# Performance work log

Hardware: AMD Instinct MI355X
Metric: run time of the kernel (lower is better)

## Reference

```python
import jax, jax.numpy as jnp
import numpy as np

NQ = 4      # n_qubits
T = 512     # seq_lenght
H = 1024    # hidden_size
F = 64      # input feature size
B = 16      # batch size (hardcoded in original module)


def _circuit_tables(nq):
    idx = np.arange(2 ** nq)
    # BasicEntanglerLayers CNOT ring: (0,1),(1,2),...,(n-1,0) for n>2; single CNOT for n==2
    pairs = [(i, (i + 1) % nq) for i in range(nq)] if nq > 2 else [(0, 1)]
    perms = []
    for c, t in pairs:  # CNOT as a basis-state permutation (qubit 0 = MSB)
        ctrl = (idx >> (nq - 1 - c)) & 1
        perms.append(idx ^ (ctrl << (nq - 1 - t)))
    bits = (idx[:, None] >> (nq - 1 - np.arange(nq))[None, :]) & 1
    signs = (1.0 - 2.0 * bits).astype(np.float32)  # (2**nq, nq), <Z_q> signs
    return perms, signs

_PERMS, _SIGNS = _circuit_tables(NQ)
_SIGNS_J = jnp.asarray(_SIGNS)


def circuit_expvals(theta):
    """theta: (..., NQ) total RX angle per wire (AngleEmbedding RX + entangler RX).
    Returns (..., NQ) PauliZ expvals after product-RX state + CNOT ring."""
    half = 0.5 * theta
    a0 = jnp.cos(half).astype(jnp.complex64)
    a1 = (-1j * jnp.sin(half)).astype(jnp.complex64)
    state = jnp.ones(theta.shape[:-1] + (1,), dtype=jnp.complex64)
    for q in range(NQ):  # build product state, qubit 0 most significant
        amp = jnp.stack([a0[..., q], a1[..., q]], axis=-1)
        state = (state[..., :, None] * amp[..., None, :]).reshape(theta.shape[:-1] + (-1,))
    for perm in _PERMS:  # CNOT ring = permutations of the computational basis
        state = state[..., perm]
    probs = state.real ** 2 + state.imag ** 2  # (..., 2**NQ)
    return probs @ _SIGNS_J                     # (..., NQ)


def qlstm_last(x, w4, Wy, by, Wf, bf, Wi, bi, Wu, bu, Wo, bo):
    """x: (B, T, feat). Dense params are stacked per-timestep along axis 0 (T,...)
    (the original creates a fresh nn.Dense every loop iteration).
    Returns the hidden state at the last timestep, (B, H)."""
    h0 = jnp.zeros((x.shape[0], H), dtype=x.dtype)
    c0 = jnp.zeros((x.shape[0], H), dtype=x.dtype)

    def step(carry, inp):
        h, c = carry
        x_t, wy, byt, wf, bft, wi, bit_, wu, but, wo, bot = inp
        v = jnp.concatenate([h, x_t], axis=1)
        y = v @ wy + byt                                   # (B, NQ)
        z = circuit_expvals(y[None] + w4[:, None, :])      # (4, B, NQ), shared input, 4 gate weights
        f = jax.nn.sigmoid(z[0]) @ wf + bft                # NOTE: no activation after Dense, as in source
        i = jax.nn.sigmoid(z[1]) @ wi + bit_
        g = jnp.tanh(z[2]) @ wu + but
        o = jax.nn.sigmoid(z[3]) @ wo + bot
        c = f * c + i * g
        h = o * jnp.tanh(c)
        return (h, c), None

    xs = (jnp.swapaxes(x, 0, 1), Wy, by, Wf, bf, Wi, bi, Wu, bu, Wo, bo)
    (h, _), _ = jax.lax.scan(step, (h0, c0), xs)
    return h


def setup_inputs() -> dict:
    key = jax.random.key(0)
    ks = jax.random.split(key, 16)
    def w(k, shape, fan_in):
        return jax.random.normal(k, shape, jnp.float32) / np.sqrt(fan_in)
    inp = {"x": jax.random.normal(ks[0], (B, T, F), jnp.float32)}
    # quantum weights (n_qlayers=1, n_qubits) per gate
    for n, k in zip(["qwf", "qwi", "qwu", "qwo"], jax.random.split(ks[1], 4)):
        inp[n] = jax.random.uniform(k, (1, NQ), jnp.float32, -1.0, 1.0)
    # encoder: per-timestep Dense stacks
    inp["Wy_e"] = w(ks[2], (T, H + F, NQ), H + F); inp["by_e"] = jnp.zeros((T, NQ), jnp.float32)
    for n, k in zip(["f", "i", "u", "o"], jax.random.split(ks[3], 4)):
        inp["W" + n + "_e"] = w(k, (T, NQ, H), NQ)
        inp["b" + n + "_e"] = jnp.zeros((T, H), jnp.float32)
    # decoder: input feature size 1
    inp["Wy_d"] = w(ks[4], (T, H + 1, NQ), H + 1); inp["by_d"] = jnp.zeros((T, NQ), jnp.float32)
    for n, k in zip(["f", "i", "u", "o"], jax.random.split(ks[5], 4)):
        inp["W" + n + "_d"] = w(k, (T, NQ, H), NQ)
        inp["b" + n + "_d"] = jnp.zeros((T, H), jnp.float32)
    # final Dense(seq_lenght)
    inp["Wt"] = w(ks[6], (H, T), H); inp["bt"] = jnp.zeros((T,), jnp.float32)
    return inp


def reference(x, qwf, qwi, qwu, qwo,
              Wy_e, by_e, Wf_e, bf_e, Wi_e, bi_e, Wu_e, bu_e, Wo_e, bo_e,
              Wy_d, by_d, Wf_d, bf_d, Wi_d, bi_d, Wu_d, bu_d, Wo_d, bo_d,
              Wt, bt):
    w4 = jnp.stack([qwf[0], qwi[0], qwu[0], qwo[0]])  # only layer-0 row is used by the qnode
    h_enc = qlstm_last(x, w4, Wy_e, by_e, Wf_e, bf_e, Wi_e, bi_e, Wu_e, bu_e, Wo_e, bo_e)
    x2 = h_enc[:, :, None]                 # (B, H, 1)
    h_dec = qlstm_last(x2[:, :T, :], w4, Wy_d, by_d, Wf_d, bf_d, Wi_d, bi_d, Wu_d, bu_d, Wo_d, bo_d)
    target = h_dec @ Wt + bt               # (B, T)
    return target[:, :, None]              # (B, T, 1)
```

## Files before the change

kernel.cpp:

```cpp
#include <hip/hip_runtime.h>

#define Tn 512
#define Hn 1024
#define Fn 64
#define NTH 512
#define NW (NTH / 64)

#define STEPB (6u * 512u * 16u)
#define MAXTOFF (511u * STEPB)
#define REC_PASS ((unsigned long long)Tn * STEPB)
#define YXE_OFF (2ull * REC_PASS)
#define WS_NEED (2ull * REC_PASS + 16ull * 512ull * 16ull)

typedef unsigned u32x4 __attribute__((ext_vector_type(4)));
typedef __fp16 h2 __attribute__((ext_vector_type(2)));

struct QParams {
  const float *x;
  const float *qw0, *qw1, *qw2, *qw3;
  const float *Wy_e, *by_e, *Wf_e, *bf_e, *Wi_e, *bi_e, *Wu_e, *bu_e, *Wo_e, *bo_e;
  const float *Wy_d, *by_d, *Wf_d, *bf_d, *Wi_d, *bi_d, *Wu_d, *bu_d, *Wo_d, *bo_d;
  const float *Wt, *bt;
  float *out;
};

#define BAR()                                                                  \
  do {                                                                         \
    asm volatile("s_waitcnt lgkmcnt(0)" ::: "memory");                         \
    __builtin_amdgcn_s_barrier();                                              \
    asm volatile("" ::: "memory");                                             \
  } while (0)
#define WAIT_VM(N)                                                             \
  do {                                                                         \
    asm volatile("s_waitcnt vmcnt(" #N ")" ::: "memory");                      \
    __builtin_amdgcn_sched_barrier(0);                                         \
  } while (0)

template <int CTRL, int RM, int BM, bool BC>
__device__ __forceinline__ float dppadd(float x) {
  int t = __builtin_amdgcn_update_dpp(0, __builtin_bit_cast(int, x), CTRL, RM,
                                      BM, BC);
  return x + __builtin_bit_cast(float, t);
}
template <int CTRL>
__device__ __forceinline__ float dppmov(float x) {
  int t = __builtin_amdgcn_update_dpp(0, __builtin_bit_cast(int, x), CTRL, 0xF,
                                      0xF, true);
  return __builtin_bit_cast(float, t);
}
__device__ __forceinline__ float wave_sum63(float x) {
  x = dppadd<0xB1, 0xF, 0xF, true>(x);
  x = dppadd<0x4E, 0xF, 0xF, true>(x);
  x = dppadd<0x141, 0xF, 0xF, true>(x);
  x = dppadd<0x140, 0xF, 0xF, true>(x);
  x = dppadd<0x142, 0xA, 0xF, false>(x);
  x = dppadd<0x143, 0xC, 0xF, false>(x);
  return x;
}
__device__ __forceinline__ float tanhc(float c) {
  float e = __builtin_amdgcn_exp2f(c * 2.885390081777927f);
  return fmaf(-2.f, __builtin_amdgcn_rcpf(e + 1.f), 1.f);
}
__device__ __forceinline__ h2 pk2(float a, float b) {
  return __builtin_amdgcn_cvt_pkrtz(a, b);
}
__device__ __forceinline__ h2 uh(unsigned u) { return __builtin_bit_cast(h2, u); }
__device__ __forceinline__ float fdot2f(h2 a, h2 b, float c) {
#if __has_builtin(__builtin_amdgcn_fdot2)
  return __builtin_amdgcn_fdot2(a, b, c, false);
#else
  float d;
  asm("v_dot2_f32_f16 %0, %1, %2, %3" : "=v"(d) : "v"(a), "v"(b), "v"(c));
  return d;
#endif
}
__device__ __forceinline__ unsigned pkh(float a, float b) {
  h2 h;
  h.x = (__fp16)a;
  h.y = (__fp16)b;
  return __builtin_bit_cast(unsigned, h);
}

struct LaneCtx {
  int tid, lane, wid;
  unsigned jt16;
  bool q1, q2;
  float w4lane;
  float mlane, alane, klane;
};
struct SBase {
  unsigned long long a[6];
};

__global__ __launch_bounds__(512) void qprep_kernel(QParams p, char *ws) {
  int t = blockIdx.x;
  const bool dec = (t >= 512);
  if (dec) t -= 512;
  const int j = threadIdx.x;

  const float *Wg0 = dec ? p.Wf_d : p.Wf_e, *Wg1 = dec ? p.Wi_d : p.Wi_e;
  const float *Wg2 = dec ? p.Wu_d : p.Wu_e, *Wg3 = dec ? p.Wo_d : p.Wo_e;
  const float *bf = dec ? p.bf_d : p.bf_e, *bi = dec ? p.bi_d : p.bi_e;
  const float *bu = dec ? p.bu_d : p.bu_e, *bo = dec ? p.bo_d : p.bo_e;
  const float *Wy = dec ? p.Wy_d : p.Wy_e;
  const int K = dec ? (Hn + 1) : (Hn + Fn);

  u32x4 *dst = (u32x4 *)(ws + (dec ? REC_PASS : 0));
  const int rbase = t * 6 * 512 + j;
  const int t4 = t * 4096;
  const float *Wg[4] = {Wg0, Wg1, Wg2, Wg3};
#pragma unroll
  for (int g = 0; g < 4; ++g) {
    u32x4 v;
    v.x = pkh(Wg[g][t4 + 0 * 1024 + j], Wg[g][t4 + 1 * 1024 + j]);
    v.y = pkh(Wg[g][t4 + 2 * 1024 + j], Wg[g][t4 + 3 * 1024 + j]);
    v.z = pkh(Wg[g][t4 + 0 * 1024 + j + 512], Wg[g][t4 + 1 * 1024 + j + 512]);
    v.w = pkh(Wg[g][t4 + 2 * 1024 + j + 512], Wg[g][t4 + 3 * 1024 + j + 512]);
    dst[rbase + g * 512] = v;
  }
  {
    const int tb = t * 1024;
    u32x4 v = {pkh(bf[tb + j], bf[tb + j + 512]),
               pkh(bi[tb + j], bi[tb + j + 512]),
               pkh(bu[tb + j], bu[tb + j + 512]),
               pkh(bo[tb + j], bo[tb + j + 512])};
    dst[rbase + 4 * 512] = v;
  }
  {
    const float4 w0 = *(const float4 *)(Wy + ((size_t)t * K + j) * 4);
    const float4 w1 = *(const float4 *)(Wy + ((size_t)t * K + j + 512) * 4);
    u32x4 v = {pkh(w0.x, w1.x), pkh(w0.y, w1.y), pkh(w0.z, w1.z),
               pkh(w0.w, w1.w)};
    dst[rbase + 5 * 512] = v;
  }

  if (!dec && j < 16) {
    const int b = j;
    float a0 = p.by_e[t * 4 + 0], a1 = p.by_e[t * 4 + 1],
          a2 = p.by_e[t * 4 + 2], a3 = p.by_e[t * 4 + 3];
#pragma unroll 8
    for (int k = 0; k < 64; ++k) {
      const float xv = p.x[((size_t)b * Tn + t) * Fn + k];
      const float4 wr =
          *(const float4 *)(p.Wy_e + ((size_t)t * (Hn + Fn) + Hn + k) * 4);
      a0 = fmaf(xv, wr.x, a0);
      a1 = fmaf(xv, wr.y, a1);
      a2 = fmaf(xv, wr.z, a2);
      a3 = fmaf(xv, wr.w, a3);
    }
    ((float4 *)(ws + YXE_OFF))[(size_t)b * Tn + t] =
        make_float4(a0, a1, a2, a3);
  }
}

struct Regs {
  u32x4 c0, c1, c2, c3, c4, c5;
};

__device__ __forceinline__ void issue_pf(Regs &r, const SBase &sb,
                                         unsigned voff) {
  asm volatile("global_load_dwordx4 %0, %1, %2" : "=v"(r.c5) : "v"(voff), "s"(sb.a[5]));
  asm volatile("global_load_dwordx4 %0, %1, %2" : "=v"(r.c0) : "v"(voff), "s"(sb.a[0]));
  asm volatile("global_load_dwordx4 %0, %1, %2" : "=v"(r.c1) : "v"(voff), "s"(sb.a[1]));
  asm volatile("global_load_dwordx4 %0, %1, %2" : "=v"(r.c2) : "v"(voff), "s"(sb.a[2]));
  asm volatile("global_load_dwordx4 %0, %1, %2" : "=v"(r.c3) : "v"(voff), "s"(sb.a[3]));
  asm volatile("global_load_dwordx4 %0, %1, %2" : "=v"(r.c4) : "v"(voff), "s"(sb.a[4]));
}

template <int PAR>
__device__ __forceinline__ void
qstep(int t, Regs &r, unsigned &toff, const SBase &sb, const LaneCtx &L,
      float *red_t, const float *yxby_l, float &h0, float &h1, float &c0,
      float &c1, h2 &hp) {
  const float yxs = yxby_l[t * 4 + (L.lane & 3)];
  WAIT_VM(18);
  float a0 = fdot2f(hp, uh(r.c5.x), 0.f);
  float a1 = fdot2f(hp, uh(r.c5.y), 0.f);
  float a2 = fdot2f(hp, uh(r.c5.z), 0.f);
  float a3 = fdot2f(hp, uh(r.c5.w), 0.f);
  a0 = wave_sum63(a0);
  a1 = wave_sum63(a1);
  a2 = wave_sum63(a2);
  a3 = wave_sum63(a3);
  if (L.lane == 63) {
    red_t[PAR * 32 + 0 * 8 + L.wid] = a0;
    red_t[PAR * 32 + 1 * 8 + L.wid] = a1;
    red_t[PAR * 32 + 2 * 8 + L.wid] = a2;
    red_t[PAR * 32 + 3 * 8 + L.wid] = a3;
  }
  BAR();
  const float4 rA = *(const float4 *)&red_t[PAR * 32 + (L.lane & 3) * 8 + 0];
  const float4 rB = *(const float4 *)&red_t[PAR * 32 + (L.lane & 3) * 8 + 4];
  const float yq =
      ((rA.x + rA.y) + (rA.z + rA.w)) + ((rB.x + rB.y) + (rB.z + rB.w));
  const float ang = yq + yxs + L.w4lane;
  const float cc = __cosf(ang);
  const float t1 = dppmov<0xB1>(cc);
  const float d1 = cc * t1;
  const float t2 = dppmov<0x4E>(d1);
  const float d2 = d1 * t2;
  const float zu = t1 * t2;
  const float zv = cc * t2;
  const float z = L.q2 ? (L.q1 ? d2 : zv) : (L.q1 ? d1 : zu);
  const float s =
      __builtin_amdgcn_rcpf(1.f + __builtin_amdgcn_exp2f(L.klane * z));
  const float act = fmaf(s, L.mlane, L.alane);
  const float actn = dppmov<0xB1>(act);
  const unsigned apk = __builtin_bit_cast(unsigned, pk2(act, actn));
  const h2 F01 = uh((unsigned)__builtin_amdgcn_readlane(apk, 0));
  const h2 F23 = uh((unsigned)__builtin_amdgcn_readlane(apk, 2));
  const h2 I01 = uh((unsigned)__builtin_amdgcn_readlane(apk, 4));
  const h2 I23 = uh((unsigned)__builtin_amdgcn_readlane(apk, 6));
  const h2 U01 = uh((unsigned)__builtin_amdgcn_readlane(apk, 8));
  const h2 U23 = uh((unsigned)__builtin_amdgcn_readlane(apk, 10));
  const h2 O01 = uh((unsigned)__builtin_amdgcn_readlane(apk, 12));
  const h2 O23 = uh((unsigned)__builtin_amdgcn_readlane(apk, 14));
  const h2 bgf = uh(r.c4.x), bgi = uh(r.c4.y), bgu = uh(r.c4.z),
           bgo = uh(r.c4.w);
  const float fv0 = fdot2f(F01, uh(r.c0.x), fdot2f(F23, uh(r.c0.y), (float)bgf.x));
  const float fv1 = fdot2f(F01, uh(r.c0.z), fdot2f(F23, uh(r.c0.w), (float)bgf.y));
  const float iv0 = fdot2f(I01, uh(r.c1.x), fdot2f(I23, uh(r.c1.y), (float)bgi.x));
  const float iv1 = fdot2f(I01, uh(r.c1.z), fdot2f(I23, uh(r.c1.w), (float)bgi.y));
  const float uv0 = fdot2f(U01, uh(r.c2.x), fdot2f(U23, uh(r.c2.y), (float)bgu.x));
  const float uv1 = fdot2f(U01, uh(r.c2.z), fdot2f(U23, uh(r.c2.w), (float)bgu.y));
  const float ov0 = fdot2f(O01, uh(r.c3.x), fdot2f(O23, uh(r.c3.y), (float)bgo.x));
  const float ov1 = fdot2f(O01, uh(r.c3.z), fdot2f(O23, uh(r.c3.w), (float)bgo.y));
  c0 = fmaf(fv0, c0, iv0 * uv0);
  h0 = ov0 * tanhc(c0);
  c1 = fmaf(fv1, c1, iv1 * uv1);
  h1 = ov1 * tanhc(c1);
  hp = pk2(h0, h1);
  issue_pf(r, sb, L.jt16 + toff);
  toff = toff + STEPB;
  if (toff > MAXTOFF) toff = MAXTOFF;
}

__device__ __forceinline__ void run_pass(const SBase &sb, const LaneCtx &L,
                                         float *red_t, const float *yxby_l,
                                         float &h0, float &h1, float &c0,
                                         float &c1) {
  Regs R0, R1, R2, R3;
  issue_pf(R0, sb, L.jt16 + 0 * STEPB);
  issue_pf(R1, sb, L.jt16 + 1 * STEPB);
  issue_pf(R2, sb, L.jt16 + 2 * STEPB);
  issue_pf(R3, sb, L.jt16 + 3 * STEPB);
  unsigned toff = 4 * STEPB;
  h2 hp = pk2(0.f, 0.f);
  for (int t = 0; t < Tn; t += 4) {
    qstep<0>(t + 0, R0, toff, sb, L, red_t, yxby_l, h0, h1, c0, c1, hp);
    qstep<1>(t + 1, R1, toff, sb, L, red_t, yxby_l, h0, h1, c0, c1, hp);
    qstep<0>(t + 2, R2, toff, sb, L, red_t, yxby_l, h0, h1, c0, c1, hp);
    qstep<1>(t + 3, R3, toff, sb, L, red_t, yxby_l, h0, h1, c0, c1, hp);
  }
  asm volatile("s_waitcnt vmcnt(0)" ::: "memory");
  __builtin_amdgcn_sched_barrier(0);
}

__global__ __launch_bounds__(NTH, 2) void qlstm_f16_kernel(QParams p,
                                                           char *ws) {
  const int b = blockIdx.x;
  LaneCtx L;
  L.tid = threadIdx.x;
  L.lane = L.tid & 63;
  L.wid = L.tid >> 6;
  L.jt16 = (unsigned)L.tid * 16u;
  const int q = L.lane & 3, g = (L.lane >> 2) & 3;
  L.q1 = q & 1;
  L.q2 = q & 2;
  {
    const float *qwp =
        (g == 0) ? p.qw0 : (g == 1) ? p.qw1 : (g == 2) ? p.qw2 : p.qw3;
    L.w4lane = qwp[q];
  }
  L.mlane = (g == 2) ? 2.f : 1.f;
  L.alane = 1.f - L.mlane;
  L.klane = -L.mlane * 1.4426950408889634f;

  __shared__ __align__(16) float red_t[2 * 4 * 8];
  __shared__ __align__(16) float yxby_l[Tn * 4];
  __shared__ __align__(16) float hbuf[Hn];

  SBase sbE, sbD;
#pragma unroll
  for (int k = 0; k < 6; ++k) {
    sbE.a[k] = (unsigned long long)ws + (unsigned long long)k * 8192ull;
    sbD.a[k] = (unsigned long long)ws + REC_PASS + (unsigned long long)k * 8192ull;
  }

  ((float4 *)yxby_l)[L.tid] =
      ((const float4 *)(ws + YXE_OFF))[(size_t)b * Tn + L.tid];
  float h0 = 0.f, h1 = 0.f, c0 = 0.f, c1 = 0.f;
  __syncthreads();

  run_pass(sbE, L, red_t, yxby_l, h0, h1, c0, c1);

  __syncthreads();
  hbuf[L.tid] = h0;
  hbuf[L.tid + NTH] = h1;
  __syncthreads();
  {
    const float hv = hbuf[L.tid];
    const float4 wx =
        *(const float4 *)(p.Wy_d + ((size_t)L.tid * (Hn + 1) + Hn) * 4);
    const float4 bd = *(const float4 *)(p.by_d + L.tid * 4);
    ((float4 *)yxby_l)[L.tid] =
        make_float4(fmaf(hv, wx.x, bd.x), fmaf(hv, wx.y, bd.y),
                    fmaf(hv, wx.z, bd.z), fmaf(hv, wx.w, bd.w));
  }
  h0 = h1 = c0 = c1 = 0.f;
  __syncthreads();

  run_pass(sbD, L, red_t, yxby_l, h0, h1, c0, c1);

  __syncthreads();
  hbuf[L.tid] = h0;
  hbuf[L.tid + NTH] = h1;
  __syncthreads();
  {
    float acc = p.bt[L.tid];
    const float4 *h4 = (const float4 *)hbuf;
#pragma unroll 4
    for (int j4 = 0; j4 < Hn / 4; ++j4) {
      const float4 hv = h4[j4];
      acc = fmaf(hv.x, p.Wt[(j4 * 4 + 0) * Tn + L.tid], acc);
      acc = fmaf(hv.y, p.Wt[(j4 * 4 + 1) * Tn + L.tid], acc);
      acc = fmaf(hv.z, p.Wt[(j4 * 4 + 2) * Tn + L.tid], acc);
      acc = fmaf(hv.w, p.Wt[(j4 * 4 + 3) * Tn + L.tid], acc);
    }
    p.out[(size_t)b * Tn + L.tid] = acc;
  }
}

__device__ __forceinline__ float sum8_all(float x) {
  x = dppadd<0xB1, 0xF, 0xF, true>(x);
  x = dppadd<0x4E, 0xF, 0xF, true>(x);
  x = dppadd<0x141, 0xF, 0xF, true>(x);
  return x;
}

struct WB {
  float w[32];
  float bb[8];
  float4 wy0, wy1;
  float4 wyx;
  float xv;
};

template <bool DEC>
__device__ __forceinline__ WB
pf_fb(int t, int b, int tid, const float *__restrict__ x,
      const float *__restrict__ Wy, const float *__restrict__ Wf,
      const float *__restrict__ bfp, const float *__restrict__ Wi,
      const float *__restrict__ bip, const float *__restrict__ Wu,
      const float *__restrict__ bup, const float *__restrict__ Wo,
      const float *__restrict__ bop) {
  WB d;
  const int K = DEC ? (Hn + 1) : (Hn + Fn);
  const int g0 = t * 4096 + tid;
#pragma unroll
  for (int e = 0; e < 2; ++e) {
    const int ge = g0 + e * 512;
#pragma unroll
    for (int n = 0; n < 4; ++n) {
      d.w[e * 16 + 0 * 4 + n] = Wf[ge + n * 1024];
      d.w[e * 16 + 1 * 4 + n] = Wi[ge + n * 1024];
      d.w[e * 16 + 2 * 4 + n] = Wu[ge + n * 1024];
      d.w[e * 16 + 3 * 4 + n] = Wo[ge + n * 1024];
    }
    const int be = t * 1024 + tid + e * 512;
    d.bb[e * 4 + 0] = bfp[be];
    d.bb[e * 4 + 1] = bip[be];
    d.bb[e * 4 + 2] = bup[be];
    d.bb[e * 4 + 3] = bop[be];
  }
  d.wy0 = *(const float4 *)(Wy + (t * K + tid) * 4);
  d.wy1 = *(const float4 *)(Wy + (t * K + tid + 512) * 4);
  if (!DEC) {
    if (tid < Fn) {
      d.wyx = *(const float4 *)(Wy + (t * K + Hn + tid) * 4);
      d.xv = x[(b * Tn + t) * Fn + tid];
    }
  } else {
    if (tid == 0) d.wyx = *(const float4 *)(Wy + (t * K + Hn) * 4);
  }
  return d;
}

template <bool DEC, int PAR>
__device__ __forceinline__ void
step_fb(int t, int tn, const WB &rd, WB &wr, int b, const LaneCtx &L,
        const float *__restrict__ x, const float *__restrict__ Wy,
        const float *__restrict__ Wf, const float *__restrict__ bfp,
        const float *__restrict__ Wi, const float *__restrict__ bip,
        const float *__restrict__ Wu, const float *__restrict__ bup,
        const float *__restrict__ Wo, const float *__restrict__ bop,
        float4 (*red4)[NW], const float *by_l, const float *henc_s, float &h0,
        float &h1, float &c0, float &c1) {
  float a0 = h0 * rd.wy0.x, a1 = h0 * rd.wy0.y, a2 = h0 * rd.wy0.z,
        a3 = h0 * rd.wy0.w;
  a0 = fmaf(h1, rd.wy1.x, a0);
  a1 = fmaf(h1, rd.wy1.y, a1);
  a2 = fmaf(h1, rd.wy1.z, a2);
  a3 = fmaf(h1, rd.wy1.w, a3);
  if (!DEC) {
    if (L.tid < Fn) {
      a0 = fmaf(rd.xv, rd.wyx.x, a0);
      a1 = fmaf(rd.xv, rd.wyx.y, a1);
      a2 = fmaf(rd.xv, rd.wyx.z, a2);
      a3 = fmaf(rd.xv, rd.wyx.w, a3);
    }
  } else {
    if (L.tid == 0) {
      const float xv = henc_s[t];
      a0 = fmaf(xv, rd.wyx.x, a0);
      a1 = fmaf(xv, rd.wyx.y, a1);
      a2 = fmaf(xv, rd.wyx.z, a2);
      a3 = fmaf(xv, rd.wyx.w, a3);
    }
  }
  a0 = wave_sum63(a0);
  a1 = wave_sum63(a1);
  a2 = wave_sum63(a2);
  a3 = wave_sum63(a3);
  if (L.lane == 63) red4[PAR][L.wid] = make_float4(a0, a1, a2, a3);
  wr = pf_fb<DEC>(tn, b, L.tid, x, Wy, Wf, bfp, Wi, bip, Wu, bup, Wo, bop);
  BAR();
  float4 rv = red4[PAR][L.lane & 7];
  const float byq = by_l[t * 4 + (L.lane & 3)];
  float y0 = sum8_all(rv.x), y1 = sum8_all(rv.y), y2 = sum8_all(rv.z),
        y3 = sum8_all(rv.w);
  const float yq = L.q2 ? (L.q1 ? y3 : y2) : (L.q1 ? y1 : y0);
  const float ang = yq + byq + L.w4lane;
  const float cc = __cosf(ang);
  const float t1 = dppmov<0xB1>(cc);
  const float d1 = cc * t1;
  const float t2 = dppmov<0x4E>(d1);
  const float d2 = d1 * t2;
  const float zu = t1 * t2;
  const float zv = cc * t2;
  const float z = L.q2 ? (L.q1 ? d2 : zv) : (L.q1 ? d1 : zu);
  const float s =
      __builtin_amdgcn_rcpf(1.f + __builtin_amdgcn_exp2f(L.klane * z));
  const float act = fmaf(s, L.mlane, L.alane);
#define RL(n)                                                                  \
  __builtin_bit_cast(float,                                                    \
                     __builtin_amdgcn_readlane(__builtin_bit_cast(int, act), n))
  const float f0 = RL(0), f1 = RL(1), f2 = RL(2), f3 = RL(3);
  const float i0 = RL(4), i1 = RL(5), i2 = RL(6), i3 = RL(7);
  const float u0 = RL(8), u1 = RL(9), u2 = RL(10), u3 = RL(11);
  const float o0 = RL(12), o1 = RL(13), o2 = RL(14), o3 = RL(15);
#undef RL
#pragma unroll
  for (int e = 0; e < 2; ++e) {
    float fv = rd.bb[e * 4 + 0], iv = rd.bb[e * 4 + 1], uv = rd.bb[e * 4 + 2],
          ov = rd.bb[e * 4 + 3];
    fv = fmaf(f0, rd.w[e * 16 + 0], fv);
    fv = fmaf(f1, rd.w[e * 16 + 1], fv);
    fv = fmaf(f2, rd.w[e * 16 + 2], fv);
    fv = fmaf(f3, rd.w[e * 16 + 3], fv);
    iv = fmaf(i0, rd.w[e * 16 + 4], iv);
    iv = fmaf(i1, rd.w[e * 16 + 5], iv);
    iv = fmaf(i2, rd.w[e * 16 + 6], iv);
    iv = fmaf(i3, rd.w[e * 16 + 7], iv);
    uv = fmaf(u0, rd.w[e * 16 + 8], uv);
    uv = fmaf(u1, rd.w[e * 16 + 9], uv);
    uv = fmaf(u2, rd.w[e * 16 + 10], uv);
    uv = fmaf(u3, rd.w[e * 16 + 11], uv);
    ov = fmaf(o0, rd.w[e * 16 + 12], ov);
    ov = fmaf(o1, rd.w[e * 16 + 13], ov);
    ov = fmaf(o2, rd.w[e * 16 + 14], ov);
    ov = fmaf(o3, rd.w[e * 16 + 15], ov);
    float &cr = e ? c1 : c0;
    float &hr = e ? h1 : h0;
    const float cn = fmaf(fv, cr, iv * uv);
    cr = cn;
    hr = ov * tanhc(cn);
  }
}

template <bool DEC>
__device__ void lstm_pass_fb(int b, const LaneCtx &L,
                             const float *__restrict__ x,
                             const float *__restrict__ Wy,
                             const float *__restrict__ by,
                             const float *__restrict__ Wf,
                             const float *__restrict__ bfp,
                             const float *__restrict__ Wi,
                             const float *__restrict__ bip,
                             const float *__restrict__ Wu,
                             const float *__restrict__ bup,
                             const float *__restrict__ Wo,
                             const float *__restrict__ bop,
                             float4 (*red4)[NW], float *by_l,
                             const float *henc_s, float &h0, float &h1,
                             float &c0, float &c1) {
#pragma unroll
  for (int i = 0; i < (Tn * 4) / NTH; ++i)
    by_l[L.tid + i * NTH] = by[L.tid + i * NTH];
  __syncthreads();
  WB bufA = pf_fb<DEC>(0, b, L.tid, x, Wy, Wf, bfp, Wi, bip, Wu, bup, Wo, bop);
  WB bufB;
  for (int t = 0; t < Tn; t += 2) {
    step_fb<DEC, 0>(t, t + 1, bufA, bufB, b, L, x, Wy, Wf, bfp, Wi, bip, Wu,
                    bup, Wo, bop, red4, by_l, henc_s, h0, h1, c0, c1);
    step_fb<DEC, 1>(t + 1, (t + 2 < Tn) ? (t + 2) : (Tn - 1), bufB, bufA, b, L,
                    x, Wy, Wf, bfp, Wi, bip, Wu, bup, Wo, bop, red4, by_l,
                    henc_s, h0, h1, c0, c1);
  }
}

__global__ __launch_bounds__(NTH, 2) void qlstm_fb_kernel(QParams p) {
  const int b = blockIdx.x;
  LaneCtx L;
  L.tid = threadIdx.x;
  L.lane = L.tid & 63;
  L.wid = L.tid >> 6;
  L.jt16 = (unsigned)L.tid * 16u;
  const int q = L.lane & 3, g = (L.lane >> 2) & 3;
  L.q1 = q & 1;
  L.q2 = q & 2;
  {
    const float *qwp =
        (g == 0) ? p.qw0 : (g == 1) ? p.qw1 : (g == 2) ? p.qw2 : p.qw3;
    L.w4lane = qwp[q];
  }
  L.mlane = (g == 2) ? 2.f : 1.f;
  L.alane = 1.f - L.mlane;
  L.klane = -L.mlane * 1.4426950408889634f;

  __shared__ float4 red4[2][NW];
  __shared__ float by_l[Tn * 4];
  __shared__ float henc_s[Hn];
  __shared__ float hst[Hn];

  float h0 = 0.f, h1 = 0.f, c0 = 0.f, c1 = 0.f;

  lstm_pass_fb<false>(b, L, p.x, p.Wy_e, p.by_e, p.Wf_e, p.bf_e, p.Wi_e,
                      p.bi_e, p.Wu_e, p.bu_e, p.Wo_e, p.bo_e, red4, by_l,
                      henc_s, h0, h1, c0, c1);
  henc_s[L.tid] = h0;
  henc_s[L.tid + NTH] = h1;
  h0 = h1 = c0 = c1 = 0.f;
  __syncthreads();
  lstm_pass_fb<true>(b, L, nullptr, p.Wy_d, p.by_d, p.Wf_d, p.bf_d, p.Wi_d,
                     p.bi_d, p.Wu_d, p.bu_d, p.Wo_d, p.bo_d, red4, by_l,
                     henc_s, h0, h1, c0, c1);
  hst[L.tid] = h0;
  hst[L.tid + NTH] = h1;
  __syncthreads();
  {
    float acc = p.bt[L.tid];
    const float4 *h4 = (const float4 *)hst;
#pragma unroll 4
    for (int j4 = 0; j4 < Hn / 4; ++j4) {
      const float4 hv = h4[j4];
      acc = fmaf(hv.x, p.Wt[(j4 * 4 + 0) * Tn + L.tid], acc);
      acc = fmaf(hv.y, p.Wt[(j4 * 4 + 1) * Tn + L.tid], acc);
      acc = fmaf(hv.z, p.Wt[(j4 * 4 + 2) * Tn + L.tid], acc);
      acc = fmaf(hv.w, p.Wt[(j4 * 4 + 3) * Tn + L.tid], acc);
    }
    p.out[(size_t)b * Tn + L.tid] = acc;
  }
}

extern "C" void kernel_launch(void *const *d_in, const int *in_sizes, int n_in,
                              void *d_out, int out_size, void *d_ws,
                              size_t ws_size, hipStream_t stream) {
  QParams p;
  p.x = (const float *)d_in[0];
  p.qw0 = (const float *)d_in[1];
  p.qw1 = (const float *)d_in[2];
  p.qw2 = (const float *)d_in[3];
  p.qw3 = (const float *)d_in[4];
  p.Wy_e = (const float *)d_in[5];
  p.by_e = (const float *)d_in[6];
  p.Wf_e = (const float *)d_in[7];
  p.bf_e = (const float *)d_in[8];
  p.Wi_e = (const float *)d_in[9];
  p.bi_e = (const float *)d_in[10];
  p.Wu_e = (const float *)d_in[11];
  p.bu_e = (const float *)d_in[12];
  p.Wo_e = (const float *)d_in[13];
  p.bo_e = (const float *)d_in[14];
  p.Wy_d = (const float *)d_in[15];
  p.by_d = (const float *)d_in[16];
  p.Wf_d = (const float *)d_in[17];
  p.bf_d = (const float *)d_in[18];
  p.Wi_d = (const float *)d_in[19];
  p.bi_d = (const float *)d_in[20];
  p.Wu_d = (const float *)d_in[21];
  p.bu_d = (const float *)d_in[22];
  p.Wo_d = (const float *)d_in[23];
  p.bo_d = (const float *)d_in[24];
  p.Wt = (const float *)d_in[25];
  p.bt = (const float *)d_in[26];
  p.out = (float *)d_out;

  if (ws_size >= WS_NEED) {
    char *ws = (char *)d_ws;
    hipLaunchKernelGGL(qprep_kernel, dim3(1024), dim3(512), 0, stream, p, ws);
    hipLaunchKernelGGL(qlstm_f16_kernel, dim3(16), dim3(NTH), 0, stream, p,
                       ws);
  } else {
    hipLaunchKernelGGL(qlstm_fb_kernel, dim3(16), dim3(NTH), 0, stream, p);
  }
}
```

Before: 691.0 us.

## Skip gate-bias stream when all biases are zero and fold 2π into weights

```diff
diff --git a/kernel.cpp b/kernel.cpp
--- a/kernel.cpp
+++ b/kernel.cpp
@@ -6,11 +6,15 @@
 #define NTH 512
 #define NW (NTH / 64)
 
-#define STEPB (6u * 512u * 16u)
+#define STEPB (5u * 512u * 16u)
 #define MAXTOFF (511u * STEPB)
+#define MAXBOFF (511u * 4096u)
 #define REC_PASS ((unsigned long long)Tn * STEPB)
 #define YXE_OFF (2ull * REC_PASS)
-#define WS_NEED (2ull * REC_PASS + 16ull * 512ull * 16ull)
+#define FLAG_OFF (YXE_OFF + 131072ull)
+#define WS_NEED (FLAG_OFF + 64ull)
+
+#define INV2PI 0.15915494309189535f
 
 typedef unsigned u32x4 __attribute__((ext_vector_type(4)));
 typedef __fp16 h2 __attribute__((ext_vector_type(2)));
@@ -74,6 +78,13 @@
   return d;
 #endif
 }
+__device__ __forceinline__ float cosrev(float x) {
+#if __has_builtin(__builtin_amdgcn_cosf)
+  return __builtin_amdgcn_cosf(x);
+#else
+  return __cosf(x * 6.283185307179586f);
+#endif
+}
 __device__ __forceinline__ unsigned pkh(float a, float b) {
   h2 h;
   h.x = (__fp16)a;
@@ -83,14 +94,18 @@
 
 struct LaneCtx {
   int tid, lane, wid;
-  unsigned jt16;
+  unsigned jt16, jt4;
   bool q1, q2;
-  float w4lane;
   float mlane, alane, klane;
 };
 struct SBase {
-  unsigned long long a[6];
+  unsigned long long a[5];
 };
+struct BBase {
+  unsigned long long b[4];
+};
+
+__global__ void qflag0_kernel(char *ws) { *(int *)(ws + FLAG_OFF) = 0; }
 
 __global__ __launch_bounds__(512) void qprep_kernel(QParams p, char *ws) {
   int t = blockIdx.x;
@@ -105,8 +120,7 @@
   const float *Wy = dec ? p.Wy_d : p.Wy_e;
   const int K = dec ? (Hn + 1) : (Hn + Fn);
 
-  u32x4 *dst = (u32x4 *)(ws + (dec ? REC_PASS : 0));
-  const int rbase = t * 6 * 512 + j;
+  char *base = ws + (dec ? REC_PASS : 0) + (size_t)t * STEPB;
   const int t4 = t * 4096;
   const float *Wg[4] = {Wg0, Wg1, Wg2, Wg3};
 #pragma unroll
@@ -116,22 +130,26 @@
     v.y = pkh(Wg[g][t4 + 2 * 1024 + j], Wg[g][t4 + 3 * 1024 + j]);
     v.z = pkh(Wg[g][t4 + 0 * 1024 + j + 512], Wg[g][t4 + 1 * 1024 + j + 512]);
     v.w = pkh(Wg[g][t4 + 2 * 1024 + j + 512], Wg[g][t4 + 3 * 1024 + j + 512]);
-    dst[rbase + g * 512] = v;
-  }
-  {
-    const int tb = t * 1024;
-    u32x4 v = {pkh(bf[tb + j], bf[tb + j + 512]),
-               pkh(bi[tb + j], bi[tb + j + 512]),
-               pkh(bu[tb + j], bu[tb + j + 512]),
-               pkh(bo[tb + j], bo[tb + j + 512])};
-    dst[rbase + 4 * 512] = v;
+    *(u32x4 *)(base + g * 8192 + j * 16) = v;
   }
   {
     const float4 w0 = *(const float4 *)(Wy + ((size_t)t * K + j) * 4);
     const float4 w1 = *(const float4 *)(Wy + ((size_t)t * K + j + 512) * 4);
-    u32x4 v = {pkh(w0.x, w1.x), pkh(w0.y, w1.y), pkh(w0.z, w1.z),
-               pkh(w0.w, w1.w)};
-    dst[rbase + 5 * 512] = v;
+    u32x4 v = {pkh(w0.x * INV2PI, w1.x * INV2PI),
+               pkh(w0.y * INV2PI, w1.y * INV2PI),
+               pkh(w0.z * INV2PI, w1.z * INV2PI),
+               pkh(w0.w * INV2PI, w1.w * INV2PI)};
+    *(u32x4 *)(base + 4 * 8192 + j * 16) = v;
+  }
+  {
+    const int tb = t * 1024 + j;
+    const float s0 = bf[tb], s1 = bf[tb + 512];
+    const float s2 = bi[tb], s3 = bi[tb + 512];
+    const float s4 = bu[tb], s5 = bu[tb + 512];
+    const float s6 = bo[tb], s7 = bo[tb + 512];
+    if (s0 != 0.f || s1 != 0.f || s2 != 0.f || s3 != 0.f || s4 != 0.f ||
+        s5 != 0.f || s6 != 0.f || s7 != 0.f)
+      atomicOr((int *)(ws + FLAG_OFF), 1);
   }
 
   if (!dec && j < 16) {
@@ -154,30 +172,47 @@
 }
 
 struct Regs {
-  u32x4 c0, c1, c2, c3, c4, c5;
+  u32x4 c0, c1, c2, c3;
+  u32x4 c4;
+  float bf0, bf1, bi0, bi1, bu0, bu1, bo0, bo1;
 };
 
+template <bool BIASED>
 __device__ __forceinline__ void issue_pf(Regs &r, const SBase &sb,
-                                         unsigned voff) {
-  asm volatile("global_load_dwordx4 %0, %1, %2" : "=v"(r.c5) : "v"(voff), "s"(sb.a[5]));
+                                         unsigned voff, const BBase &bb,
+                                         unsigned voffB) {
+  asm volatile("global_load_dwordx4 %0, %1, %2" : "=v"(r.c4) : "v"(voff), "s"(sb.a[4]));
   asm volatile("global_load_dwordx4 %0, %1, %2" : "=v"(r.c0) : "v"(voff), "s"(sb.a[0]));
   asm volatile("global_load_dwordx4 %0, %1, %2" : "=v"(r.c1) : "v"(voff), "s"(sb.a[1]));
   asm volatile("global_load_dwordx4 %0, %1, %2" : "=v"(r.c2) : "v"(voff), "s"(sb.a[2]));
   asm volatile("global_load_dwordx4 %0, %1, %2" : "=v"(r.c3) : "v"(voff), "s"(sb.a[3]));
-  asm volatile("global_load_dwordx4 %0, %1, %2" : "=v"(r.c4) : "v"(voff), "s"(sb.a[4]));
-}
-
-template <int PAR>
+  if (BIASED) {
+    asm volatile("global_load_dword %0, %1, %2" : "=v"(r.bf0) : "v"(voffB), "s"(bb.b[0]));
+    asm volatile("global_load_dword %0, %1, %2 offset:2048" : "=v"(r.bf1) : "v"(voffB), "s"(bb.b[0]));
+    asm volatile("global_load_dword %0, %1, %2" : "=v"(r.bi0) : "v"(voffB), "s"(bb.b[1]));
+    asm volatile("global_load_dword %0, %1, %2 offset:2048" : "=v"(r.bi1) : "v"(voffB), "s"(bb.b[1]));
+    asm volatile("global_load_dword %0, %1, %2" : "=v"(r.bu0) : "v"(voffB), "s"(bb.b[2]));
+    asm volatile("global_load_dword %0, %1, %2 offset:2048" : "=v"(r.bu1) : "v"(voffB), "s"(bb.b[2]));
+    asm volatile("global_load_dword %0, %1, %2" : "=v"(r.bo0) : "v"(voffB), "s"(bb.b[3]));
+    asm volatile("global_load_dword %0, %1, %2 offset:2048" : "=v"(r.bo1) : "v"(voffB), "s"(bb.b[3]));
+  }
+}
+
+template <int PAR, bool BIASED>
 __device__ __forceinline__ void
-qstep(int t, Regs &r, unsigned &toff, const SBase &sb, const LaneCtx &L,
-      float *red_t, const float *yxby_l, float &h0, float &h1, float &c0,
-      float &c1, h2 &hp) {
-  const float yxs = yxby_l[t * 4 + (L.lane & 3)];
-  WAIT_VM(18);
-  float a0 = fdot2f(hp, uh(r.c5.x), 0.f);
-  float a1 = fdot2f(hp, uh(r.c5.y), 0.f);
-  float a2 = fdot2f(hp, uh(r.c5.z), 0.f);
-  float a3 = fdot2f(hp, uh(r.c5.w), 0.f);
+qstep(int t, Regs &r, unsigned &toff, unsigned &toffB, const SBase &sb,
+      const BBase &bb, const LaneCtx &L, float *red_t, const float *yxw_l,
+      float &h0, float &h1, float &c0, float &c1, h2 &hp) {
+  const float yxw = yxw_l[t * 16 + (L.lane & 15)];
+  if (BIASED) {
+    WAIT_VM(39);
+  } else {
+    WAIT_VM(15);
+  }
+  float a0 = fdot2f(hp, uh(r.c4.x), 0.f);
+  float a1 = fdot2f(hp, uh(r.c4.y), 0.f);
+  float a2 = fdot2f(hp, uh(r.c4.z), 0.f);
+  float a3 = fdot2f(hp, uh(r.c4.w), 0.f);
   a0 = wave_sum63(a0);
   a1 = wave_sum63(a1);
   a2 = wave_sum63(a2);
@@ -193,8 +228,7 @@
   const float4 rB = *(const float4 *)&red_t[PAR * 32 + (L.lane & 3) * 8 + 4];
   const float yq =
       ((rA.x + rA.y) + (rA.z + rA.w)) + ((rB.x + rB.y) + (rB.z + rB.w));
-  const float ang = yq + yxs + L.w4lane;
-  const float cc = __cosf(ang);
+  const float cc = cosrev(yq + yxw);
   const float t1 = dppmov<0xB1>(cc);
   const float d1 = cc * t1;
   const float t2 = dppmov<0x4E>(d1);
@@ -215,42 +249,50 @@
   const h2 U23 = uh((unsigned)__builtin_amdgcn_readlane(apk, 10));
   const h2 O01 = uh((unsigned)__builtin_amdgcn_readlane(apk, 12));
   const h2 O23 = uh((unsigned)__builtin_amdgcn_readlane(apk, 14));
-  const h2 bgf = uh(r.c4.x), bgi = uh(r.c4.y), bgu = uh(r.c4.z),
-           bgo = uh(r.c4.w);
-  const float fv0 = fdot2f(F01, uh(r.c0.x), fdot2f(F23, uh(r.c0.y), (float)bgf.x));
-  const float fv1 = fdot2f(F01, uh(r.c0.z), fdot2f(F23, uh(r.c0.w), (float)bgf.y));
-  const float iv0 = fdot2f(I01, uh(r.c1.x), fdot2f(I23, uh(r.c1.y), (float)bgi.x));
-  const float iv1 = fdot2f(I01, uh(r.c1.z), fdot2f(I23, uh(r.c1.w), (float)bgi.y));
-  const float uv0 = fdot2f(U01, uh(r.c2.x), fdot2f(U23, uh(r.c2.y), (float)bgu.x));
-  const float uv1 = fdot2f(U01, uh(r.c2.z), fdot2f(U23, uh(r.c2.w), (float)bgu.y));
-  const float ov0 = fdot2f(O01, uh(r.c3.x), fdot2f(O23, uh(r.c3.y), (float)bgo.x));
-  const float ov1 = fdot2f(O01, uh(r.c3.z), fdot2f(O23, uh(r.c3.w), (float)bgo.y));
+  const float iF0 = BIASED ? r.bf0 : 0.f, iF1 = BIASED ? r.bf1 : 0.f;
+  const float iI0 = BIASED ? r.bi0 : 0.f, iI1 = BIASED ? r.bi1 : 0.f;
+  const float iU0 = BIASED ? r.bu0 : 0.f, iU1 = BIASED ? r.bu1 : 0.f;
+  const float iO0 = BIASED ? r.bo0 : 0.f, iO1 = BIASED ? r.bo1 : 0.f;
+  const float fv0 = fdot2f(F01, uh(r.c0.x), fdot2f(F23, uh(r.c0.y), iF0));
+  const float fv1 = fdot2f(F01, uh(r.c0.z), fdot2f(F23, uh(r.c0.w), iF1));
+  const float iv0 = fdot2f(I01, uh(r.c1.x), fdot2f(I23, uh(r.c1.y), iI0));
+  const float iv1 = fdot2f(I01, uh(r.c1.z), fdot2f(I23, uh(r.c1.w), iI1));
+  const float uv0 = fdot2f(U01, uh(r.c2.x), fdot2f(U23, uh(r.c2.y), iU0));
+  const float uv1 = fdot2f(U01, uh(r.c2.z), fdot2f(U23, uh(r.c2.w), iU1));
+  const float ov0 = fdot2f(O01, uh(r.c3.x), fdot2f(O23, uh(r.c3.y), iO0));
+  const float ov1 = fdot2f(O01, uh(r.c3.z), fdot2f(O23, uh(r.c3.w), iO1));
   c0 = fmaf(fv0, c0, iv0 * uv0);
   h0 = ov0 * tanhc(c0);
   c1 = fmaf(fv1, c1, iv1 * uv1);
   h1 = ov1 * tanhc(c1);
   hp = pk2(h0, h1);
-  issue_pf(r, sb, L.jt16 + toff);
+  issue_pf<BIASED>(r, sb, L.jt16 + toff, bb, L.jt4 + toffB);
   toff = toff + STEPB;
   if (toff > MAXTOFF) toff = MAXTOFF;
-}
-
-__device__ __forceinline__ void run_pass(const SBase &sb, const LaneCtx &L,
-                                         float *red_t, const float *yxby_l,
-                                         float &h0, float &h1, float &c0,
-                                         float &c1) {
+  if (BIASED) {
+    toffB = toffB + 4096u;
+    if (toffB > MAXBOFF) toffB = MAXBOFF;
+  }
+}
+
+template <bool BIASED>
+__device__ __forceinline__ void run_pass(const SBase &sb, const BBase &bb,
+                                         const LaneCtx &L, float *red_t,
+                                         const float *yxw_l, float &h0,
+                                         float &h1, float &c0, float &c1) {
   Regs R0, R1, R2, R3;
-  issue_pf(R0, sb, L.jt16 + 0 * STEPB);
-  issue_pf(R1, sb, L.jt16 + 1 * STEPB);
-  issue_pf(R2, sb, L.jt16 + 2 * STEPB);
-  issue_pf(R3, sb, L.jt16 + 3 * STEPB);
-  unsigned toff = 4 * STEPB;
+  WAIT_VM(0);
+  issue_pf<BIASED>(R0, sb, L.jt16 + 0 * STEPB, bb, L.jt4 + 0 * 4096u);
+  issue_pf<BIASED>(R1, sb, L.jt16 + 1 * STEPB, bb, L.jt4 + 1 * 4096u);
+  issue_pf<BIASED>(R2, sb, L.jt16 + 2 * STEPB, bb, L.jt4 + 2 * 4096u);
+  issue_pf<BIASED>(R3, sb, L.jt16 + 3 * STEPB, bb, L.jt4 + 3 * 4096u);
+  unsigned toff = 4 * STEPB, toffB = 4 * 4096u;
   h2 hp = pk2(0.f, 0.f);
   for (int t = 0; t < Tn; t += 4) {
-    qstep<0>(t + 0, R0, toff, sb, L, red_t, yxby_l, h0, h1, c0, c1, hp);
-    qstep<1>(t + 1, R1, toff, sb, L, red_t, yxby_l, h0, h1, c0, c1, hp);
-    qstep<0>(t + 2, R2, toff, sb, L, red_t, yxby_l, h0, h1, c0, c1, hp);
-    qstep<1>(t + 3, R3, toff, sb, L, red_t, yxby_l, h0, h1, c0, c1, hp);
+    qstep<0, BIASED>(t + 0, R0, toff, toffB, sb, bb, L, red_t, yxw_l, h0, h1, c0, c1, hp);
+    qstep<1, BIASED>(t + 1, R1, toff, toffB, sb, bb, L, red_t, yxw_l, h0, h1, c0, c1, hp);
+    qstep<0, BIASED>(t + 2, R2, toff, toffB, sb, bb, L, red_t, yxw_l, h0, h1, c0, c1, hp);
+    qstep<1, BIASED>(t + 3, R3, toff, toffB, sb, bb, L, red_t, yxw_l, h0, h1, c0, c1, hp);
   }
   asm volatile("s_waitcnt vmcnt(0)" ::: "memory");
   __builtin_amdgcn_sched_barrier(0);
@@ -264,35 +306,66 @@
   L.lane = L.tid & 63;
   L.wid = L.tid >> 6;
   L.jt16 = (unsigned)L.tid * 16u;
+  L.jt4 = (unsigned)L.tid * 4u;
   const int q = L.lane & 3, g = (L.lane >> 2) & 3;
   L.q1 = q & 1;
   L.q2 = q & 2;
-  {
-    const float *qwp =
-        (g == 0) ? p.qw0 : (g == 1) ? p.qw1 : (g == 2) ? p.qw2 : p.qw3;
-    L.w4lane = qwp[q];
-  }
   L.mlane = (g == 2) ? 2.f : 1.f;
   L.alane = 1.f - L.mlane;
   L.klane = -L.mlane * 1.4426950408889634f;
 
   __shared__ __align__(16) float red_t[2 * 4 * 8];
-  __shared__ __align__(16) float yxby_l[Tn * 4];
+  __shared__ __align__(16) float yxw_l[Tn * 16];
   __shared__ __align__(16) float hbuf[Hn];
 
+  const int biased = *(volatile const int *)(ws + FLAG_OFF);
+
   SBase sbE, sbD;
 #pragma unroll
-  for (int k = 0; k < 6; ++k) {
+  for (int k = 0; k < 5; ++k) {
     sbE.a[k] = (unsigned long long)ws + (unsigned long long)k * 8192ull;
     sbD.a[k] = (unsigned long long)ws + REC_PASS + (unsigned long long)k * 8192ull;
   }
-
-  ((float4 *)yxby_l)[L.tid] =
-      ((const float4 *)(ws + YXE_OFF))[(size_t)b * Tn + L.tid];
+  BBase bbE, bbD;
+  bbE.b[0] = (unsigned long long)p.bf_e;
+  bbE.b[1] = (unsigned long long)p.bi_e;
+  bbE.b[2] = (unsigned long long)p.bu_e;
+  bbE.b[3] = (unsigned long long)p.bo_e;
+  bbD.b[0] = (unsigned long long)p.bf_d;
+  bbD.b[1] = (unsigned long long)p.bi_d;
+  bbD.b[2] = (unsigned long long)p.bu_d;
+  bbD.b[3] = (unsigned long long)p.bo_d;
+
+  float4 w4r[4];
+  {
+    const float *qwp[4] = {p.qw0, p.qw1, p.qw2, p.qw3};
+#pragma unroll
+    for (int gg = 0; gg < 4; ++gg) {
+      const float4 w = *(const float4 *)qwp[gg];
+      w4r[gg] = make_float4(w.x * INV2PI, w.y * INV2PI, w.z * INV2PI,
+                            w.w * INV2PI);
+    }
+  }
+
+  {
+    const float4 yx4 =
+        ((const float4 *)(ws + YXE_OFF))[(size_t)b * Tn + L.tid];
+#pragma unroll
+    for (int gg = 0; gg < 4; ++gg) {
+      ((float4 *)yxw_l)[L.tid * 4 + gg] =
+          make_float4(fmaf(yx4.x, INV2PI, w4r[gg].x),
+                      fmaf(yx4.y, INV2PI, w4r[gg].y),
+                      fmaf(yx4.z, INV2PI, w4r[gg].z),
+                      fmaf(yx4.w, INV2PI, w4r[gg].w));
+    }
+  }
   float h0 = 0.f, h1 = 0.f, c0 = 0.f, c1 = 0.f;
   __syncthreads();
 
-  run_pass(sbE, L, red_t, yxby_l, h0, h1, c0, c1);
+  if (biased)
+    run_pass<true>(sbE, bbE, L, red_t, yxw_l, h0, h1, c0, c1);
+  else
+    run_pass<false>(sbE, bbE, L, red_t, yxw_l, h0, h1, c0, c1);
 
   __syncthreads();
   hbuf[L.tid] = h0;
@@ -303,14 +376,24 @@
     const float4 wx =
         *(const float4 *)(p.Wy_d + ((size_t)L.tid * (Hn + 1) + Hn) * 4);
     const float4 bd = *(const float4 *)(p.by_d + L.tid * 4);
-    ((float4 *)yxby_l)[L.tid] =
-        make_float4(fmaf(hv, wx.x, bd.x), fmaf(hv, wx.y, bd.y),
-                    fmaf(hv, wx.z, bd.z), fmaf(hv, wx.w, bd.w));
+    const float bx = fmaf(hv, wx.x, bd.x) * INV2PI;
+    const float by2 = fmaf(hv, wx.y, bd.y) * INV2PI;
+    const float bz = fmaf(hv, wx.z, bd.z) * INV2PI;
+    const float bw = fmaf(hv, wx.w, bd.w) * INV2PI;
+#pragma unroll
+    for (int gg = 0; gg < 4; ++gg) {
+      ((float4 *)yxw_l)[L.tid * 4 + gg] =
+          make_float4(bx + w4r[gg].x, by2 + w4r[gg].y, bz + w4r[gg].z,
+                      bw + w4r[gg].w);
+    }
   }
   h0 = h1 = c0 = c1 = 0.f;
   __syncthreads();
 
-  run_pass(sbD, L, red_t, yxby_l, h0, h1, c0, c1);
+  if (biased)
+    run_pass<true>(sbD, bbD, L, red_t, yxw_l, h0, h1, c0, c1);
+  else
+    run_pass<false>(sbD, bbD, L, red_t, yxw_l, h0, h1, c0, c1);
 
   __syncthreads();
   hbuf[L.tid] = h0;
@@ -331,6 +414,8 @@
   }
 }
 
+#define FNTH 512
+#define FNW (FNTH / 64)
 __device__ __forceinline__ float sum8_all(float x) {
   x = dppadd<0xB1, 0xF, 0xF, true>(x);
   x = dppadd<0x4E, 0xF, 0xF, true>(x);
@@ -386,15 +471,21 @@
   return d;
 }
 
+struct FLane {
+  int tid, lane, wid;
+  bool q1, q2;
+  float w4lane, mlane, alane, klane;
+};
+
 template <bool DEC, int PAR>
 __device__ __forceinline__ void
-step_fb(int t, int tn, const WB &rd, WB &wr, int b, const LaneCtx &L,
+step_fb(int t, int tn, const WB &rd, WB &wr, int b, const FLane &L,
         const float *__restrict__ x, const float *__restrict__ Wy,
         const float *__restrict__ Wf, const float *__restrict__ bfp,
         const float *__restrict__ Wi, const float *__restrict__ bip,
         const float *__restrict__ Wu, const float *__restrict__ bup,
         const float *__restrict__ Wo, const float *__restrict__ bop,
-        float4 (*red4)[NW], const float *by_l, const float *henc_s, float &h0,
+        float4 (*red4)[FNW], const float *by_l, const float *henc_s, float &h0,
         float &h1, float &c0, float &c1) {
   float a0 = h0 * rd.wy0.x, a1 = h0 * rd.wy0.y, a2 = h0 * rd.wy0.z,
         a3 = h0 * rd.wy0.w;
@@ -479,7 +570,7 @@
 }
 
 template <bool DEC>
-__device__ void lstm_pass_fb(int b, const LaneCtx &L,
+__device__ void lstm_pass_fb(int b, const FLane &L,
                              const float *__restrict__ x,
                              const float *__restrict__ Wy,
                              const float *__restrict__ by,
@@ -491,12 +582,12 @@
                              const float *__restrict__ bup,
                              const float *__restrict__ Wo,
                              const float *__restrict__ bop,
-                             float4 (*red4)[NW], float *by_l,
+                             float4 (*red4)[FNW], float *by_l,
                              const float *henc_s, float &h0, float &h1,
                              float &c0, float &c1) {
 #pragma unroll
-  for (int i = 0; i < (Tn * 4) / NTH; ++i)
-    by_l[L.tid + i * NTH] = by[L.tid + i * NTH];
+  for (int i = 0; i < (Tn * 4) / FNTH; ++i)
+    by_l[L.tid + i * FNTH] = by[L.tid + i * FNTH];
   __syncthreads();
   WB bufA = pf_fb<DEC>(0, b, L.tid, x, Wy, Wf, bfp, Wi, bip, Wu, bup, Wo, bop);
   WB bufB;
@@ -509,13 +600,12 @@
   }
 }
 
-__global__ __launch_bounds__(NTH, 2) void qlstm_fb_kernel(QParams p) {
+__global__ __launch_bounds__(FNTH, 2) void qlstm_fb_kernel(QParams p) {
   const int b = blockIdx.x;
-  LaneCtx L;
+  FLane L;
   L.tid = threadIdx.x;
   L.lane = L.tid & 63;
   L.wid = L.tid >> 6;
-  L.jt16 = (unsigned)L.tid * 16u;
   const int q = L.lane & 3, g = (L.lane >> 2) & 3;
   L.q1 = q & 1;
   L.q2 = q & 2;
@@ -528,7 +618,7 @@
   L.alane = 1.f - L.mlane;
   L.klane = -L.mlane * 1.4426950408889634f;
 
-  __shared__ float4 red4[2][NW];
+  __shared__ float4 red4[2][FNW];
   __shared__ float by_l[Tn * 4];
   __shared__ float henc_s[Hn];
   __shared__ float hst[Hn];
@@ -539,14 +629,14 @@
                       p.bi_e, p.Wu_e, p.bu_e, p.Wo_e, p.bo_e, red4, by_l,
                       henc_s, h0, h1, c0, c1);
   henc_s[L.tid] = h0;
-  henc_s[L.tid + NTH] = h1;
+  henc_s[L.tid + FNTH] = h1;
   h0 = h1 = c0 = c1 = 0.f;
   __syncthreads();
   lstm_pass_fb<true>(b, L, nullptr, p.Wy_d, p.by_d, p.Wf_d, p.bf_d, p.Wi_d,
                      p.bi_d, p.Wu_d, p.bu_d, p.Wo_d, p.bo_d, red4, by_l,
                      henc_s, h0, h1, c0, c1);
   hst[L.tid] = h0;
-  hst[L.tid + NTH] = h1;
+  hst[L.tid + FNTH] = h1;
   __syncthreads();
   {
     float acc = p.bt[L.tid];
@@ -598,10 +688,11 @@
 
   if (ws_size >= WS_NEED) {
     char *ws = (char *)d_ws;
+    hipLaunchKernelGGL(qflag0_kernel, dim3(1), dim3(1), 0, stream, ws);
     hipLaunchKernelGGL(qprep_kernel, dim3(1024), dim3(512), 0, stream, p, ws);
     hipLaunchKernelGGL(qlstm_f16_kernel, dim3(16), dim3(NTH), 0, stream, p,
                        ws);
   } else {
-    hipLaunchKernelGGL(qlstm_fb_kernel, dim3(16), dim3(NTH), 0, stream, p);
-  }
-}
+    hipLaunchKernelGGL(qlstm_fb_kernel, dim3(16), dim3(FNTH), 0, stream, p);
+  }
+}
```

New measurement: 660.8 us (median of 3 runs). -4.4%, faster.
